# Kernel optimization log

Measured on AMD Instinct MI355X. Metric: run time of the kernel, lower is better.

## Reference

```python
import jax, jax.numpy as jnp
import numpy as np

H = 1024      # hidden_size
NH = 16       # num_heads
HD = H // NH  # head_dim
FF = 4 * H    # ffn hidden


def setup_inputs() -> dict:
    key = jax.random.key(0)
    ks = jax.random.split(key, 11)
    s = 1.0 / np.sqrt(H)
    inp = {
        "x": jax.random.normal(ks[0], (2, 2048, H), dtype=jnp.float32),
        "Wq": jax.random.uniform(ks[1], (H, H), jnp.float32, -s, s),
        "Wk": jax.random.uniform(ks[2], (H, H), jnp.float32, -s, s),
        "Wv": jax.random.uniform(ks[3], (H, H), jnp.float32, -s, s),
        "Wo": jax.random.uniform(ks[4], (H, H), jnp.float32, -s, s),
        "ln1_g": jnp.ones((H,), jnp.float32),
        "ln1_b": jnp.zeros((H,), jnp.float32),
        "ln2_g": jnp.ones((H,), jnp.float32),
        "ln2_b": jnp.zeros((H,), jnp.float32),
        "W1": jax.random.uniform(ks[5], (H, FF), jnp.float32, -s, s),
        "b1": jnp.zeros((FF,), jnp.float32),
        "W2": jax.random.uniform(ks[6], (FF, H), jnp.float32, -1.0 / np.sqrt(FF), 1.0 / np.sqrt(FF)),
        "b2": jnp.zeros((H,), jnp.float32),
    }
    return inp


def _layernorm(x, g, b, eps=1e-5):
    mu = jnp.mean(x, axis=-1, keepdims=True)
    var = jnp.mean(jnp.square(x - mu), axis=-1, keepdims=True)
    return (x - mu) * jax.lax.rsqrt(var + eps) * g + b


def reference(x, Wq, Wk, Wv, Wo, ln1_g, ln1_b, ln2_g, ln2_b, W1, b1, W2, b2):
    bsz, seq, _ = x.shape
    h = _layernorm(x, ln1_g, ln1_b)
    # project and split heads: [b, s, H] -> [b, nh, s, hd]
    def split(t):
        return t.reshape(bsz, seq, NH, HD).transpose(0, 2, 1, 3)
    q = split(h @ Wq.T)
    k = split(h @ Wk.T)
    v = split(h @ Wv.T)
    scores = jnp.einsum("bhqd,bhkd->bhqk", q, k) / jnp.sqrt(jnp.float32(HD))
    probs = jax.nn.softmax(scores, axis=-1)
    attn = jnp.einsum("bhqk,bhkd->bhqd", probs, v)
    attn = attn.transpose(0, 2, 1, 3).reshape(bsz, seq, H)
    x = x + attn @ Wo.T
    h2 = _layernorm(x, ln2_g, ln2_b)
    ffn = jax.nn.gelu(h2 @ W1 + b1, approximate=False) @ W2 + b2
    return x + ffn
```

## Files before the change

### kernel.cpp

```cpp
#include <hip/hip_runtime.h>
#include <stdint.h>
#include <math.h>

typedef float f32x4 __attribute__((ext_vector_type(4)));
typedef __bf16 bf16x8 __attribute__((ext_vector_type(8)));

#define DEVI __device__ __forceinline__

#if __has_builtin(__builtin_amdgcn_exp2f)
#define EXP2(x) __builtin_amdgcn_exp2f(x)
#else
#define EXP2(x) exp2f(x)
#endif

#define LOG2E 1.44269504f

DEVI unsigned short f2bf(float f) {
  union { float f; unsigned int u; } c; c.f = f;
  unsigned int u = c.u;
  return (unsigned short)((u + 0x7FFFu + ((u >> 16) & 1u)) >> 16);
}

DEVI unsigned short f2bf_fast(float f) {
  union { float f; unsigned int u; } c; c.f = f;
  return (unsigned short)((c.u + 0x8000u) >> 16);
}

DEVI void gll16(const void* g, void* l) {
  __builtin_amdgcn_global_load_lds(
      (const __attribute__((address_space(1))) void*)g,
      (__attribute__((address_space(3))) void*)l,
      16, 0, 0);
}

__global__ __launch_bounds__(256) void cvt_weights(
    const float* __restrict__ Wq, const float* __restrict__ Wk,
    const float* __restrict__ Wv, const float* __restrict__ Wo,
    unsigned short* __restrict__ WB, unsigned short* __restrict__ WoB) {
  int i = blockIdx.x * 256 + threadIdx.x;
  int seg = i >> 18;
  int j = i & 262143;
  const float* src = (seg == 0) ? Wq : (seg == 1) ? Wk : (seg == 2) ? Wv : Wo;
  unsigned short* dst = (seg < 3) ? WB + (size_t)seg * 1048576 : WoB;
  float4 v = ((const float4*)src)[j];
  ushort4 ov;
  ov.x = f2bf(v.x); ov.y = f2bf(v.y); ov.z = f2bf(v.z); ov.w = f2bf(v.w);
  ((ushort4*)dst)[j] = ov;
}

__global__ __launch_bounds__(256) void transpose_f32_bf16(
    const float* __restrict__ in, unsigned short* __restrict__ out, int R, int C) {
  __shared__ float tile[32][33];
  int bc = blockIdx.x * 32, br = blockIdx.y * 32;
  int tx = threadIdx.x & 31, ty = threadIdx.x >> 5;
#pragma unroll
  for (int i = 0; i < 32; i += 8)
    tile[ty + i][tx] = in[(size_t)(br + ty + i) * C + bc + tx];
  __syncthreads();
#pragma unroll
  for (int i = 0; i < 32; i += 8)
    out[(size_t)(bc + ty + i) * R + br + tx] = f2bf(tile[tx][ty + i]);
}

__global__ __launch_bounds__(256) void vtrans(
    const unsigned short* __restrict__ QKV, unsigned short* __restrict__ Vt) {
  int stile = blockIdx.x;
  int bh = blockIdx.y;
  int b = bh >> 4, h = bh & 15;
  __shared__ unsigned short tile[64][68];
  const unsigned short* src =
      QKV + ((size_t)(b * 2048 + stile * 64)) * 3072 + 2048 + h * 64;
  int t = threadIdx.x;
#pragma unroll
  for (int i = 0; i < 16; i++) {
    int e = i * 256 + t; int s = e >> 6, d = e & 63;
    tile[s][d] = src[(size_t)s * 3072 + d];
  }
  __syncthreads();
  unsigned short* dst = Vt + (size_t)bh * 64 * 2048 + stile * 64;
#pragma unroll
  for (int i = 0; i < 16; i++) {
    int e = i * 256 + t; int d = e >> 6, s = e & 63;
    dst[(size_t)d * 2048 + s] = tile[s][d];
  }
}

__global__ __launch_bounds__(256) void layernorm_bf16(
    const float* __restrict__ x, const float* __restrict__ g,
    const float* __restrict__ be, unsigned short* __restrict__ out) {
  const int row = blockIdx.x;
  const int t = threadIdx.x;
  const float4 v = ((const float4*)(x + (size_t)row * 1024))[t];
  float s = v.x + v.y + v.z + v.w;
  float s2 = v.x * v.x + v.y * v.y + v.z * v.z + v.w * v.w;
#pragma unroll
  for (int d = 32; d > 0; d >>= 1) {
    s += __shfl_down(s, d);
    s2 += __shfl_down(s2, d);
  }
  __shared__ float ps[4], ps2[4], st[2];
  const int lane = t & 63, wave = t >> 6;
  if (lane == 0) { ps[wave] = s; ps2[wave] = s2; }
  __syncthreads();
  if (t == 0) {
    float S = ps[0] + ps[1] + ps[2] + ps[3];
    float S2 = ps2[0] + ps2[1] + ps2[2] + ps2[3];
    float mu = S * (1.0f / 1024.0f);
    float var = S2 * (1.0f / 1024.0f) - mu * mu;
    st[0] = mu; st[1] = rsqrtf(var + 1e-5f);
  }
  __syncthreads();
  float mu = st[0], inv = st[1];
  float4 gv = ((const float4*)g)[t];
  float4 bv = ((const float4*)be)[t];
  ushort4 ov;
  ov.x = f2bf((v.x - mu) * inv * gv.x + bv.x);
  ov.y = f2bf((v.y - mu) * inv * gv.y + bv.y);
  ov.z = f2bf((v.z - mu) * inv * gv.z + bv.z);
  ov.w = f2bf((v.w - mu) * inv * gv.w + bv.w);
  ((ushort4*)(out + (size_t)row * 1024))[t] = ov;
}

DEVI float gelu_f(float x) {
  float a = x * (2.3022082f + 0.1029432f * x * x);
  return x / (1.0f + EXP2(-a));
}

template <int EPI>
__global__ __launch_bounds__(512, 4) void gemm_bt8(
    const unsigned short* __restrict__ A, const unsigned short* __restrict__ B,
    int M, int N, int K, unsigned short* __restrict__ outB,
    const float* __restrict__ bias) {
  __shared__ __align__(16) unsigned short As[2][128 * 32];
  __shared__ __align__(16) unsigned short Bs[2][128 * 32];
  const int t = threadIdx.x;
  const int lane = t & 63, wave = t >> 6;
  const int wm = wave >> 2, wn = wave & 3;
  const int l15 = lane & 15, lg = lane >> 4;
  const int sl = (t & 7) ^ ((t >> 3) & 7);
  const int srow2 = ((t >> 3) << 1) + (sl >> 2);
  const int scol2 = (sl & 3) * 8;
  const int gx = gridDim.x;
  const int nwg = gx * gridDim.y;
  const int orig = blockIdx.y * gx + blockIdx.x;
  const int swz = (orig & 7) * (nwg >> 3) + (orig >> 3);
  const int bx = swz % gx, by = swz / gx;
  const size_t aBase = (size_t)by * 128 * K;
  const size_t bBase = (size_t)bx * 128 * K;
  f32x4 acc[4][2] = {};

  auto stage = [&](int buf, int kt) {
    gll16(A + aBase + (size_t)srow2 * K + kt + scol2, (char*)&As[buf][0] + t * 16);
    gll16(B + bBase + (size_t)srow2 * K + kt + scol2, (char*)&Bs[buf][0] + t * 16);
  };

  stage(0, 0);
  __syncthreads();
  const int nk = K >> 5;
  for (int ki = 0; ki < nk; ki++) {
    const int cur = ki & 1;
    if (ki + 1 < nk) stage(cur ^ 1, (ki + 1) << 5);
    bf16x8 af[4], bfv[2];
#pragma unroll
    for (int m = 0; m < 4; m++) {
      const int R = wm * 64 + m * 16 + l15;
      const int r = R >> 1;
      const int ps = (((R & 1) << 2) | lg) ^ (r & 7);
      af[m] = *(const bf16x8*)&As[cur][r * 64 + ps * 8];
    }
#pragma unroll
    for (int n = 0; n < 2; n++) {
      const int R = wn * 32 + n * 16 + l15;
      const int r = R >> 1;
      const int ps = (((R & 1) << 2) | lg) ^ (r & 7);
      bfv[n] = *(const bf16x8*)&Bs[cur][r * 64 + ps * 8];
    }
#pragma unroll
    for (int m = 0; m < 4; m++)
#pragma unroll
      for (int n = 0; n < 2; n++)
        acc[m][n] = __builtin_amdgcn_mfma_f32_16x16x32_bf16(af[m], bfv[n], acc[m][n], 0, 0, 0);
    __syncthreads();
  }
  const int rowB = by * 128 + wm * 64;
  const int colB = bx * 128 + wn * 32;
#pragma unroll
  for (int m = 0; m < 4; m++) {
#pragma unroll
    for (int n = 0; n < 2; n++) {
      const int gn = colB + n * 16 + l15;
      float bb = (EPI == 2) ? bias[gn] : 0.0f;
#pragma unroll
      for (int r = 0; r < 4; r++) {
        const int gm = rowB + m * 16 + lg * 4 + r;
        const size_t idx = (size_t)gm * N + gn;
        if (EPI == 0) outB[idx] = f2bf(acc[m][n][r]);
        else          outB[idx] = f2bf(gelu_f(acc[m][n][r] + bb));
      }
    }
  }
}

template <int EPI, int TM, int TN>
__global__ __launch_bounds__(256, 4) void gemm_bt(
    const unsigned short* __restrict__ A, const unsigned short* __restrict__ B,
    int M, int N, int K, float* __restrict__ outF,
    const float* __restrict__ res, const float* __restrict__ bias) {
  __shared__ __align__(16) unsigned short As[2][TM * 32];
  __shared__ __align__(16) unsigned short Bs[2][TN * 32];
  constexpr int MF = TM / 32;
  constexpr int NF = TN / 32;
  const int t = threadIdx.x;
  const int lane = t & 63, wave = t >> 6;
  const int wr = wave >> 1, wc = wave & 1;
  const int l15 = lane & 15, lg = lane >> 4;
  const int sl = (t & 7) ^ ((t >> 3) & 7);
  const int srow2 = ((t >> 3) << 1) + (sl >> 2);
  const int scol2 = (sl & 3) * 8;
  const int gx = gridDim.x;
  const int nwg = gx * gridDim.y;
  const int orig = blockIdx.y * gx + blockIdx.x;
  const int swz = (orig & 7) * (nwg >> 3) + (orig >> 3);
  const int bx = swz % gx, by = swz / gx;
  const size_t aBase = (size_t)by * TM * K;
  const size_t bBase = (size_t)bx * TN * K;
  f32x4 acc[MF][NF] = {};

  auto stage = [&](int buf, int kt) {
#pragma unroll
    for (int i = 0; i < TM / 64; i++)
      gll16(A + aBase + (size_t)(srow2 + i * 64) * K + kt + scol2,
            (char*)&As[buf][0] + i * 4096 + t * 16);
#pragma unroll
    for (int i = 0; i < TN / 64; i++)
      gll16(B + bBase + (size_t)(srow2 + i * 64) * K + kt + scol2,
            (char*)&Bs[buf][0] + i * 4096 + t * 16);
  };

  stage(0, 0);
  __syncthreads();
  const int nk = K >> 5;
  for (int ki = 0; ki < nk; ki++) {
    const int cur = ki & 1;
    if (ki + 1 < nk) stage(cur ^ 1, (ki + 1) << 5);
    bf16x8 af[MF], bfv[NF];
#pragma unroll
    for (int m = 0; m < MF; m++) {
      const int R = wr * (TM / 2) + m * 16 + l15;
      const int r = R >> 1;
      const int ps = (((R & 1) << 2) | lg) ^ (r & 7);
      af[m] = *(const bf16x8*)&As[cur][r * 64 + ps * 8];
    }
#pragma unroll
    for (int n = 0; n < NF; n++) {
      const int R = wc * (TN / 2) + n * 16 + l15;
      const int r = R >> 1;
      const int ps = (((R & 1) << 2) | lg) ^ (r & 7);
      bfv[n] = *(const bf16x8*)&Bs[cur][r * 64 + ps * 8];
    }
#pragma unroll
    for (int m = 0; m < MF; m++)
#pragma unroll
      for (int n = 0; n < NF; n++)
        acc[m][n] = __builtin_amdgcn_mfma_f32_16x16x32_bf16(af[m], bfv[n], acc[m][n], 0, 0, 0);
    __syncthreads();
  }
  const int rowB = by * TM + wr * (TM / 2);
  const int colB = bx * TN + wc * (TN / 2);
#pragma unroll
  for (int m = 0; m < MF; m++) {
#pragma unroll
    for (int n = 0; n < NF; n++) {
#pragma unroll
      for (int r = 0; r < 4; r++) {
        int gm = rowB + m * 16 + lg * 4 + r;
        int gn = colB + n * 16 + l15;
        float c = acc[m][n][r];
        size_t idx = (size_t)gm * N + gn;
        if (EPI == 1) outF[idx] = res[idx] + c;
        else          outF[idx] = res[idx] + c + bias[gn];
      }
    }
  }
}

__global__ __launch_bounds__(512) void attn_flash(
    const unsigned short* __restrict__ QKV, const unsigned short* __restrict__ Vt,
    unsigned short* __restrict__ attnO) {
  __shared__ __align__(16) unsigned short Ks[2][64 * 64];
  __shared__ __align__(16) unsigned short Vs[2][64 * 64];
  __shared__ __align__(16) unsigned short Ps[128 * 64];
  const int t = threadIdx.x;
  const int lane = t & 63, wave = t >> 6;
  const int l15 = lane & 15, lg = lane >> 4;
  const int bid = blockIdx.x;
  const int swzb = (bid & 7) * 64 + (bid >> 3);
  const int qt = swzb & 15;
  const int bh = swzb >> 4;
  const int b = bh >> 4, h = bh & 15;
  const size_t qkvBase = (size_t)b * 2048 * 3072 + (size_t)h * 64;

  bf16x8 aq[2];
  {
    int qrow = qt * 128 + wave * 16 + l15;
    const unsigned short* qp = QKV + qkvBase + (size_t)qrow * 3072;
#pragma unroll
    for (int kc = 0; kc < 2; kc++) {
      aq[kc] = *(const bf16x8*)(qp + kc * 32 + lg * 8);
#pragma unroll
      for (int j = 0; j < 8; j++)
        aq[kc][j] = (__bf16)((float)aq[kc][j] * 0.125f);
    }
  }
  bf16x8 onesf;
#pragma unroll
  for (int j = 0; j < 8; j++) onesf[j] = (__bf16)1.0f;

  const unsigned short* Kg = QKV + qkvBase + 1024;
  const unsigned short* Vg = Vt + (size_t)bh * 64 * 2048;

  f32x4 o[4] = {};
  f32x4 ol = {};
  const float M2 = 4.0f * LOG2E;

  const int srow = t >> 3;
  const int scb = (t & 7) * 16;
  const int e = (scb ^ ((srow & 7) << 4)) >> 1;

  auto stage = [&](int buf, int kt) {
    gll16(Kg + (size_t)(kt * 64 + srow) * 3072 + e, (char*)&Ks[buf][0] + t * 16);
    gll16(Vg + (size_t)srow * 2048 + kt * 64 + e, (char*)&Vs[buf][0] + t * 16);
  };

  stage(0, 0);
  __syncthreads();

  for (int kt = 0; kt < 32; kt++) {
    const int cur = kt & 1;
    if (kt < 31) stage(cur ^ 1, kt + 1);

    f32x4 s[4] = {};
#pragma unroll
    for (int n = 0; n < 4; n++) {
#pragma unroll
      for (int kc = 0; kc < 2; kc++) {
        int r = n * 16 + l15;
        int cb = (kc * 64 + lg * 16) ^ ((r & 7) << 4);
        bf16x8 bk = *(const bf16x8*)&Ks[cur][r * 64 + (cb >> 1)];
        s[n] = __builtin_amdgcn_mfma_f32_16x16x32_bf16(aq[kc], bk, s[n], 0, 0, 0);
      }
    }

    const int q0 = wave * 16 + lg * 4;
#pragma unroll
    for (int n = 0; n < 4; n++)
#pragma unroll
      for (int r = 0; r < 4; r++) {
        int q = q0 + r;
        int cb = ((n * 16 + l15) * 2) ^ ((q & 7) << 4);
        float p = EXP2(__builtin_fmaf(s[n][r], LOG2E, -M2));
        Ps[q * 64 + (cb >> 1)] = f2bf_fast(p);
      }

#pragma unroll
    for (int kc = 0; kc < 2; kc++) {
      int qr = wave * 16 + l15;
      int cbp = (kc * 64 + lg * 16) ^ ((qr & 7) << 4);
      bf16x8 pa = *(const bf16x8*)&Ps[qr * 64 + (cbp >> 1)];
      ol = __builtin_amdgcn_mfma_f32_16x16x32_bf16(pa, onesf, ol, 0, 0, 0);
#pragma unroll
      for (int n = 0; n < 4; n++) {
        int dr = n * 16 + l15;
        int cbv = (kc * 64 + lg * 16) ^ ((dr & 7) << 4);
        bf16x8 bv = *(const bf16x8*)&Vs[cur][dr * 64 + (cbv >> 1)];
        o[n] = __builtin_amdgcn_mfma_f32_16x16x32_bf16(pa, bv, o[n], 0, 0, 0);
      }
    }
    __syncthreads();
  }

  const int qrow0 = qt * 128 + wave * 16;
  unsigned short* op = attnO + ((size_t)(b * 2048 + qrow0)) * 1024 + h * 64;
  float inv[4];
#pragma unroll
  for (int r = 0; r < 4; r++) inv[r] = 1.0f / ol[r];
#pragma unroll
  for (int n = 0; n < 4; n++)
#pragma unroll
    for (int r = 0; r < 4; r++) {
      int q = lg * 4 + r;
      op[(size_t)q * 1024 + n * 16 + l15] = f2bf(o[n][r] * inv[r]);
    }
}

extern "C" void kernel_launch(void* const* d_in, const int* in_sizes, int n_in,
                              void* d_out, int out_size, void* d_ws, size_t ws_size,
                              hipStream_t stream) {
  const float* x = (const float*)d_in[0];
  const float* Wq = (const float*)d_in[1];
  const float* Wk = (const float*)d_in[2];
  const float* Wv = (const float*)d_in[3];
  const float* Wo = (const float*)d_in[4];
  const float* ln1g = (const float*)d_in[5];
  const float* ln1b = (const float*)d_in[6];
  const float* ln2g = (const float*)d_in[7];
  const float* ln2b = (const float*)d_in[8];
  const float* W1 = (const float*)d_in[9];
  const float* b1 = (const float*)d_in[10];
  const float* W2 = (const float*)d_in[11];
  const float* b2 = (const float*)d_in[12];
  float* out = (float*)d_out;

  char* ws = (char*)d_ws;
  size_t off = 0;
  auto alloc = [&](size_t bytes) {
    void* p = ws + off;
    off += (bytes + 255) & ~(size_t)255;
    return p;
  };
  unsigned short* WB = (unsigned short*)alloc(3072ull * 1024 * 2);
  unsigned short* WoB = (unsigned short*)alloc(1024ull * 1024 * 2);
  unsigned short* W1t = (unsigned short*)alloc(4096ull * 1024 * 2);
  unsigned short* W2t = (unsigned short*)alloc(1024ull * 4096 * 2);
  unsigned short* hb = (unsigned short*)alloc(4096ull * 1024 * 2);
  unsigned short* QKV = (unsigned short*)alloc(4096ull * 3072 * 2);
  unsigned short* attnb = (unsigned short*)alloc(4096ull * 1024 * 2);
  unsigned short* Vtb = (unsigned short*)alloc(32ull * 64 * 2048 * 2);
  float* x2 = (float*)alloc(4096ull * 1024 * 4);
  unsigned short* ffnb = QKV;
  unsigned short* h2b = hb;

  cvt_weights<<<4096, 256, 0, stream>>>(Wq, Wk, Wv, Wo, WB, WoB);
  transpose_f32_bf16<<<dim3(128, 32), 256, 0, stream>>>(W1, W1t, 1024, 4096);
  transpose_f32_bf16<<<dim3(32, 128), 256, 0, stream>>>(W2, W2t, 4096, 1024);
  layernorm_bf16<<<4096, 256, 0, stream>>>(x, ln1g, ln1b, hb);
  gemm_bt8<0><<<dim3(24, 32), 512, 0, stream>>>(hb, WB, 4096, 3072, 1024,
                                                QKV, nullptr);
  vtrans<<<dim3(32, 32), 256, 0, stream>>>(QKV, Vtb);
  attn_flash<<<512, 512, 0, stream>>>(QKV, Vtb, attnb);
  gemm_bt<1, 64, 128><<<dim3(8, 64), 256, 0, stream>>>(attnb, WoB, 4096, 1024, 1024,
                                                       x2, x, nullptr);
  layernorm_bf16<<<4096, 256, 0, stream>>>(x2, ln2g, ln2b, h2b);
  gemm_bt8<2><<<dim3(32, 32), 512, 0, stream>>>(h2b, W1t, 4096, 4096, 1024,
                                                ffnb, b1);
  gemm_bt<3, 64, 128><<<dim3(8, 64), 256, 0, stream>>>(ffnb, W2t, 4096, 1024, 4096,
                                                       out, x2, b2);
}
```

Baseline: 245.7 us.

## Split attention over two key halves and merge partial outputs in a new kernel

The flash attention kernel now splits the key/value sequence into two halves, so twice as many blocks are launched. Each block writes its unnormalized partial output in bf16 and its row sums to a workspace that reuses the x2 buffer. A new merge kernel adds the two partials, divides by the combined sum and writes the attention output. This aims to fill the GPU better than the old 512-block grid could, at the cost of an extra launch, extra memory traffic, and bf16 rounding of the unnormalized partials.

```diff
diff --git a/kernel.cpp b/kernel.cpp
--- a/kernel.cpp
+++ b/kernel.cpp
@@ -19,6 +19,10 @@
   union { float f; unsigned int u; } c; c.f = f;
   unsigned int u = c.u;
   return (unsigned short)((u + 0x7FFFu + ((u >> 16) & 1u)) >> 16);
+}
+DEVI float bf2f(unsigned short h) {
+  union { unsigned int u; float f; } c; c.u = ((unsigned int)h) << 16;
+  return c.f;
 }
 
 DEVI unsigned short f2bf_fast(float f) {
@@ -286,7 +290,7 @@
 
 __global__ __launch_bounds__(512) void attn_flash(
     const unsigned short* __restrict__ QKV, const unsigned short* __restrict__ Vt,
-    unsigned short* __restrict__ attnO) {
+    unsigned short* __restrict__ opart, float* __restrict__ lpart) {
   __shared__ __align__(16) unsigned short Ks[2][64 * 64];
   __shared__ __align__(16) unsigned short Vs[2][64 * 64];
   __shared__ __align__(16) unsigned short Ps[128 * 64];
@@ -294,11 +298,14 @@
   const int lane = t & 63, wave = t >> 6;
   const int l15 = lane & 15, lg = lane >> 4;
   const int bid = blockIdx.x;
-  const int swzb = (bid & 7) * 64 + (bid >> 3);
+  const int half = bid & 1;
+  const int sub = bid >> 1;
+  const int swzb = (sub & 7) * 64 + (sub >> 3);
   const int qt = swzb & 15;
   const int bh = swzb >> 4;
   const int b = bh >> 4, h = bh & 15;
   const size_t qkvBase = (size_t)b * 2048 * 3072 + (size_t)h * 64;
+  const int kt0 = half * 16;
 
   bf16x8 aq[2];
   {
@@ -332,12 +339,12 @@
     gll16(Vg + (size_t)srow * 2048 + kt * 64 + e, (char*)&Vs[buf][0] + t * 16);
   };
 
-  stage(0, 0);
-  __syncthreads();
-
-  for (int kt = 0; kt < 32; kt++) {
-    const int cur = kt & 1;
-    if (kt < 31) stage(cur ^ 1, kt + 1);
+  stage(0, kt0);
+  __syncthreads();
+
+  for (int i = 0; i < 16; i++) {
+    const int cur = i & 1;
+    if (i < 15) stage(cur ^ 1, kt0 + i + 1);
 
     f32x4 s[4] = {};
 #pragma unroll
@@ -380,17 +387,42 @@
   }
 
   const int qrow0 = qt * 128 + wave * 16;
-  unsigned short* op = attnO + ((size_t)(b * 2048 + qrow0)) * 1024 + h * 64;
-  float inv[4];
-#pragma unroll
-  for (int r = 0; r < 4; r++) inv[r] = 1.0f / ol[r];
+  unsigned short* op = opart + (size_t)half * 4096 * 1024 +
+                       ((size_t)(b * 2048 + qrow0)) * 1024 + h * 64;
 #pragma unroll
   for (int n = 0; n < 4; n++)
 #pragma unroll
     for (int r = 0; r < 4; r++) {
       int q = lg * 4 + r;
-      op[(size_t)q * 1024 + n * 16 + l15] = f2bf(o[n][r] * inv[r]);
-    }
+      op[(size_t)q * 1024 + n * 16 + l15] = f2bf(o[n][r]);
+    }
+  if (l15 == 0) {
+#pragma unroll
+    for (int r = 0; r < 4; r++) {
+      int row = b * 2048 + qrow0 + lg * 4 + r;
+      lpart[half * 65536 + row * 16 + h] = ol[r];
+    }
+  }
+}
+
+__global__ __launch_bounds__(256) void attn_merge(
+    const unsigned short* __restrict__ opart, const float* __restrict__ lpart,
+    unsigned short* __restrict__ attnb) {
+  const int row = blockIdx.x;
+  const int t = threadIdx.x;
+  const int d0 = t * 4;
+  const int h = d0 >> 6;
+  const float l = lpart[row * 16 + h] + lpart[65536 + row * 16 + h];
+  const float inv = 1.0f / l;
+  const size_t idx = (size_t)row * 1024 + d0;
+  ushort4 o1 = *(const ushort4*)(opart + idx);
+  ushort4 o2 = *(const ushort4*)(opart + 4194304 + idx);
+  ushort4 ov;
+  ov.x = f2bf((bf2f(o1.x) + bf2f(o2.x)) * inv);
+  ov.y = f2bf((bf2f(o1.y) + bf2f(o2.y)) * inv);
+  ov.z = f2bf((bf2f(o1.z) + bf2f(o2.z)) * inv);
+  ov.w = f2bf((bf2f(o1.w) + bf2f(o2.w)) * inv);
+  *(ushort4*)(attnb + idx) = ov;
 }
 
 extern "C" void kernel_launch(void* const* d_in, const int* in_sizes, int n_in,
@@ -427,8 +459,10 @@
   unsigned short* attnb = (unsigned short*)alloc(4096ull * 1024 * 2);
   unsigned short* Vtb = (unsigned short*)alloc(32ull * 64 * 2048 * 2);
   float* x2 = (float*)alloc(4096ull * 1024 * 4);
+  float* lpart = (float*)alloc(2ull * 4096 * 16 * 4);
   unsigned short* ffnb = QKV;
   unsigned short* h2b = hb;
+  unsigned short* opart = (unsigned short*)x2;
 
   cvt_weights<<<4096, 256, 0, stream>>>(Wq, Wk, Wv, Wo, WB, WoB);
   transpose_f32_bf16<<<dim3(128, 32), 256, 0, stream>>>(W1, W1t, 1024, 4096);
@@ -437,7 +471,8 @@
   gemm_bt8<0><<<dim3(24, 32), 512, 0, stream>>>(hb, WB, 4096, 3072, 1024,
                                                 QKV, nullptr);
   vtrans<<<dim3(32, 32), 256, 0, stream>>>(QKV, Vtb);
-  attn_flash<<<512, 512, 0, stream>>>(QKV, Vtb, attnb);
+  attn_flash<<<1024, 512, 0, stream>>>(QKV, Vtb, opart, lpart);
+  attn_merge<<<4096, 256, 0, stream>>>(opart, lpart, attnb);
   gemm_bt<1, 64, 128><<<dim3(8, 64), 256, 0, stream>>>(attnb, WoB, 4096, 1024, 1024,
                                                        x2, x, nullptr);
   layernorm_bf16<<<4096, 256, 0, stream>>>(x2, ln2g, ln2b, h2b);
```

After: 253.1 us. 3.0% more time.
